# Performance work log

Measured on AMD Instinct MI355X. Metric: run time of the kernel, lower is better.

## Reference

```python
import jax, jax.numpy as jnp
import numpy as np

B = 8          # batch_size
N = 2048       # N_particles
D_SP = 2       # spatial dims
D = 16         # D_SP + hidden_dim
K = 32         # max_num_neighbors
R = 0.08       # neighbor_radius
DT = 0.01      # leapfrog step
BIG = 1e9


def setup_inputs() -> dict:
    key = jax.random.key(0)
    ks = jax.random.split(key, 8)
    H, C = 64, 32
    # node state: small random hidden features, deterministic disk positions
    x = jax.random.normal(ks[0], (B * N, D), dtype=jnp.float32) * 0.001
    i = jnp.arange(N, dtype=jnp.float32)
    golden = jnp.pi * (3.0 - jnp.sqrt(5.0))
    theta = i * golden
    r = 0.6 * jnp.sqrt((i + 0.5) / N)
    pos = jnp.stack([r * jnp.cos(theta), r * jnp.sin(theta)], axis=1)  # [N,2]
    pos = jnp.tile(pos, (B, 1)) + 0.01 * jax.random.normal(ks[1], (B * N, 2), dtype=jnp.float32)
    x = x.at[:, :D_SP].set(pos)
    W1 = jax.random.normal(ks[2], (2 * D, H), dtype=jnp.float32) * (1.0 / np.sqrt(2 * D))
    b1 = jnp.zeros((H,), jnp.float32)
    W2 = jax.random.normal(ks[3], (H, C), dtype=jnp.float32) * (1.0 / np.sqrt(H))
    b2 = jnp.zeros((C,), jnp.float32)
    Wout = jax.random.normal(ks[4], (C, 1), dtype=jnp.float32) * (1.0 / np.sqrt(C))
    bout = jnp.zeros((1,), jnp.float32)
    batch = jnp.repeat(jnp.arange(B, dtype=jnp.int64), N)
    return {"x": x, "W1": W1, "b1": b1, "W2": W2, "b2": b2,
            "Wout": Wout, "bout": bout, "batch": batch, "steps": 2}


def reference(x, W1, b1, W2, b2, Wout, bout, batch, steps):
    Bn, Df = x.shape
    Bc = int(np.asarray(batch)[-1]) + 1      # batch is contiguous blocks
    Nn = Bn // Bc
    eye = jnp.eye(Nn, dtype=x.dtype) * BIG   # no self-loops (loop=False)

    def hamiltonian(xv):
        xb = xv.reshape(Bc, Nn, Df)
        pos = xb[:, :, :D_SP]                              # [B,N,2]
        # radius_graph: pairwise sq-dist per simulation, capped at K neighbors
        d2 = jnp.sum((pos[:, :, None, :] - pos[:, None, :, :]) ** 2, axis=-1)  # [B,N,N]
        d2 = d2 + eye
        negd, idx = jax.lax.top_k(-d2, K)                  # K nearest per node
        valid = (-negd) < (R * R)                          # [B,N,K]
        # gather neighbor states (HNNConv message on concat(x_i, x_j))
        xj = xb[jnp.arange(Bc)[:, None, None], idx]        # [B,N,K,D]
        xi = jnp.broadcast_to(xb[:, :, None, :], xj.shape)
        m = jnp.tanh(jnp.concatenate([xi, xj], axis=-1) @ W1 + b1)  # [B,N,K,H]
        m = m @ W2 + b2                                    # [B,N,K,C]
        m = jnp.where(valid[..., None], m, 0.0)
        agg = m.sum(axis=2)                                # sum aggregation [B,N,C]
        h = agg @ Wout + bout                              # per-node Hamiltonian [B,N,1]
        return h.sum()

    for _ in range(int(steps)):
        dHdx = jax.grad(hamiltonian)(x)
        x = x - DT * dHdx
    return x
```

## Files before the change

### kernel.cpp

```cpp
#include <hip/hip_runtime.h>
#include <cstdint>
#include <cstddef>

#define BB   8
#define NN   2048
#define DD   16
#define HHH  64
#define KK   32
#define CAP  96
#define FCAP 48
#define DT_C 0.01f
#define R2_C (0.08f * 0.08f)
#define CEXP (-2.885390081777927f)

#define GRID 17
#define NCEL (GRID * GRID)
#define GOFF 0.68f
#define CINV 12.5f
#define CSTRIDE 320

#define WPB   8
#define BLOCK (WPB * 64)

__device__ __forceinline__ float dist2(float px, float py, float qx, float qy) {
    float dx = __fsub_rn(px, qx);
    float dy = __fsub_rn(py, qy);
    return __fadd_rn(__fmul_rn(dx, dx), __fmul_rn(dy, dy));
}

__device__ __forceinline__ int prefix_cnt(unsigned long long m) {
    return (int)__builtin_amdgcn_mbcnt_hi(
        (unsigned)(m >> 32), __builtin_amdgcn_mbcnt_lo((unsigned)m, 0u));
}

__device__ __forceinline__ int swizzled_slot(int blk, int w, int& bbase) {
    bbase = (blk & 7) << 11;
    return (blk >> 3) * WPB + w;
}

__device__ __forceinline__ int clampi(int v, int lo, int hi) {
    return v < lo ? lo : (v > hi ? hi : v);
}

template <bool FIRST>
__global__ __launch_bounds__(1024) void k_bin(
    const float* __restrict__ x, const float* __restrict__ pos,
    const float* __restrict__ W2, const float* __restrict__ Wout,
    float2* __restrict__ sortedPos, unsigned short* __restrict__ sortedIdx,
    int* __restrict__ cellStart, float* __restrict__ vOut) {
    __shared__ int hist[NCEL], base[NCEL + 1], cursor[NCEL];
    int bat = blockIdx.x, bbase = bat << 11, tid = threadIdx.x;
    if (tid < NCEL) hist[tid] = 0;
    if (blockIdx.x == 0 && tid >= 512 && tid < 512 + HHH) {
        int hh = tid - 512;
        float acc = 0.f;
        for (int c = 0; c < 32; c++) acc = fmaf(W2[hh * 32 + c], Wout[c], acc);
        vOut[hh] = acc;
    }
    __syncthreads();
    float2 q[2]; int cid[2];
#pragma unroll
    for (int u = 0; u < 2; ++u) {
        int i = tid + (u << 10);
        float2 qq = FIRST ? *(const float2*)(x + (size_t)(bbase + i) * DD)
                          : *(const float2*)(pos + (size_t)(bbase + i) * 2);
        q[u] = qq;
        int cx = clampi((int)((qq.x + GOFF) * CINV), 0, GRID - 1);
        int cy = clampi((int)((qq.y + GOFF) * CINV), 0, GRID - 1);
        cid[u] = cy * GRID + cx;
        atomicAdd(&hist[cid[u]], 1);
    }
    __syncthreads();
    if (tid < 64) {
        int loc[5], s = 0;
#pragma unroll
        for (int k = 0; k < 5; ++k) {
            int idx = tid * 5 + k;
            loc[k] = (idx < NCEL) ? hist[idx] : 0;
            s += loc[k];
        }
        int pre = s;
#pragma unroll
        for (int off = 1; off < 64; off <<= 1) {
            int t = __shfl_up(pre, off);
            if (tid >= off) pre += t;
        }
        pre -= s;
#pragma unroll
        for (int k = 0; k < 5; ++k) {
            int idx = tid * 5 + k;
            if (idx <= NCEL) base[idx] = pre;
            pre += loc[k];
        }
    }
    __syncthreads();
    if (tid < NCEL) cursor[tid] = base[tid];
    if (tid <= NCEL) cellStart[bat * CSTRIDE + tid] = base[tid];
    __syncthreads();
#pragma unroll
    for (int u = 0; u < 2; ++u) {
        int dst = atomicAdd(&cursor[cid[u]], 1);
        sortedPos[bbase + dst] = q[u];
        sortedIdx[bbase + dst] = (unsigned short)(tid + (u << 10));
    }
}

__global__ __launch_bounds__(BLOCK) void k_neighbors(
    const float* __restrict__ x,
    const float2* __restrict__ sortedPos, const unsigned short* __restrict__ sortedIdx,
    const int* __restrict__ cellStart, const float* __restrict__ W1,
    float2* __restrict__ candList, unsigned short* __restrict__ fwdList,
    int* __restrict__ cntArr, float* __restrict__ cutArr,
    float* __restrict__ Aplane, float* __restrict__ Dplane) {
    __shared__ float2 sDJ[WPB][CAP];

    int tid = threadIdx.x;
    int w = tid >> 6, lane = tid & 63;
    int bbase;
    int s = swizzled_slot(blockIdx.x, w, bbase);
    int bat = bbase >> 11;
    int gs = bbase + s;

    int jol = (int)sortedIdx[gs];
    const float* xrow = x + (size_t)(bbase + jol) * DD;
    float xv = (lane < DD) ? xrow[lane] : 0.f;
    float px = __shfl(xv, 0), py = __shfl(xv, 1);
    float A = 0.f, Dv = 0.f;
#pragma unroll
    for (int f = 0; f < DD; f++) {
        float xf = __shfl(xv, f);
        A  = fmaf(xf, W1[f * HHH + lane], A);
        Dv = fmaf(xf, W1[(DD + f) * HHH + lane], Dv);
    }
    Aplane[((size_t)gs << 6) + lane] = A;
    Dplane[((size_t)gs << 6) + lane] = Dv;

    const int* CS = cellStart + bat * CSTRIDE;
    int cx = clampi((int)((px + GOFF) * CINV), 0, GRID - 1);
    int cy = clampi((int)((py + GOFF) * CINV), 0, GRID - 1);
    int xlo = cx > 0 ? cx - 1 : 0;
    int xhi = cx < GRID - 1 ? cx + 1 : GRID - 1;
    int rs0 = 0, rl0 = 0, rs1 = 0, rl1 = 0, rs2 = 0, rl2 = 0;
    if (cy > 0) {
        int a = CS[(cy - 1) * GRID + xlo], b = CS[(cy - 1) * GRID + xhi + 1];
        rs0 = a; rl0 = b - a;
    }
    {
        int a = CS[cy * GRID + xlo], b = CS[cy * GRID + xhi + 1];
        rs1 = a; rl1 = b - a;
    }
    if (cy < GRID - 1) {
        int a = CS[(cy + 1) * GRID + xlo], b = CS[(cy + 1) * GRID + xhi + 1];
        rs2 = a; rl2 = b - a;
    }
    int tot = rl0 + rl1 + rl2;

    int cnt = 0;
    for (int c0 = 0; c0 < tot; c0 += 64) {
        int t = c0 + lane;
        int j = rs0 + t;
        int u1 = t - rl0;
        if (u1 >= 0) j = rs1 + u1;
        int u2 = u1 - rl1;
        if (u2 >= 0) j = rs2 + u2;
        bool in = t < tot;
        float2 q = sortedPos[bbase + (in ? j : 0)];
        float d2 = dist2(px, py, q.x, q.y);
        bool hit = in && (d2 < R2_C);
        unsigned long long m = __ballot(hit);
        int idx = cnt + prefix_cnt(m);
        if (hit && idx < CAP)
            sDJ[w][idx] = make_float2(d2, __uint_as_float((unsigned)j));
        cnt += (int)__popcll(m);
    }
    if (cnt > CAP) cnt = CAP;
    __threadfence_block();

    float cutoff = R2_C;
    if (cnt > KK + 1) {
        const float INF = 1e30f;
        if (cnt <= 64) {
            float v = (lane < cnt) ? sDJ[w][lane].x : INF;
#pragma unroll
            for (int k = 2; k <= 64; k <<= 1) {
#pragma unroll
                for (int j = k >> 1; j > 0; j >>= 1) {
                    float pv = __shfl_xor(v, j);
                    bool up = ((lane & k) == 0);
                    bool takeMin = (((lane & j) == 0) == up);
                    v = takeMin ? fminf(v, pv) : fmaxf(v, pv);
                }
            }
            cutoff = __shfl(v, KK);
        } else {
            float e0 = (lane < cnt) ? sDJ[w][lane].x : INF;
            float e1 = (lane + 64 < cnt) ? sDJ[w][lane + 64].x : INF;
            int r0 = 0, q0 = 0, r1 = 0, q1 = 0;
            for (int k = 0; k < cnt; k++) {
                float val = sDJ[w][k].x;
                r0 += (val < e0); q0 += (val == e0);
                r1 += (val < e1); q1 += (val == e1);
            }
            bool c0 = (r0 <= KK) && (r0 + q0 > KK);
            bool c1 = (r1 <= KK) && (r1 + q1 > KK);
            float cand = c0 ? e0 : (c1 ? e1 : INF);
#pragma unroll
            for (int off = 32; off; off >>= 1) cand = fminf(cand, __shfl_xor(cand, off));
            cutoff = cand;
        }
    }

    int me = 0, mf = 0;
    for (int c0 = 0; c0 < cnt; c0 += 64) {
        int c = c0 + lane;
        bool act = c < cnt;
        float2 e = sDJ[w][act ? c : 0];
        unsigned js = __float_as_uint(e.y);
        bool keep = act && ((int)js != s);
        unsigned long long mK = __ballot(keep);
        int ie = me + prefix_cnt(mK);
        if (keep) candList[(size_t)gs * CAP + ie] = e;
        me += (int)__popcll(mK);
        bool fw = keep && (e.x <= cutoff);
        unsigned long long mF = __ballot(fw);
        int iF = mf + prefix_cnt(mF);
        if (fw && iF < FCAP) fwdList[(size_t)gs * FCAP + iF] = (unsigned short)js;
        mf += (int)__popcll(mF);
    }
    if (mf > FCAP) mf = FCAP;
    if (lane == 0) { cutArr[gs] = cutoff; cntArr[gs] = me | (mf << 16); }
}

__global__ __launch_bounds__(BLOCK) void k_grad(
    const float* __restrict__ x, const unsigned short* __restrict__ sortedIdx,
    const float* __restrict__ cutArr, const int* __restrict__ cntArr,
    const float2* __restrict__ candList, const unsigned short* __restrict__ fwdList,
    const float* __restrict__ Aplane, const float* __restrict__ Dplane,
    const float* __restrict__ W1, const float* __restrict__ b1,
    const float* __restrict__ vArr,
    float* __restrict__ xOut, float* __restrict__ posOut) {
    __shared__ float sW1t[HHH * 33];
    __shared__ alignas(16) unsigned short sFwd[WPB][FCAP];
    __shared__ alignas(16) unsigned short sRev[WPB][CAP];
    __shared__ float sS[WPB][128];

    int tid = threadIdx.x;
    int w = tid >> 6, h = tid & 63;
    int bbase;
    int s = swizzled_slot(blockIdx.x, w, bbase);
    int gs = bbase + s;

    for (int t = tid; t < 2 * DD * HHH; t += BLOCK) {
        int f = t >> 6, hh = t & 63;
        sW1t[hh * 33 + f] = W1[t];
    }
    __syncthreads();

    float b1h = b1[h];
    float Apb = Aplane[((size_t)gs << 6) + h] + b1h;
    float Dpb = Dplane[((size_t)gs << 6) + h] + b1h;
    float vh4 = 4.f * vArr[h];
    int packed = cntArr[gs];
    int cnt = packed & 0xffff;
    int mf = packed >> 16;

    if (h < mf) sFwd[w][h] = fwdList[(size_t)gs * FCAP + h];

    int mr = 0;
    for (int c0 = 0; c0 < cnt; c0 += 64) {
        int c = c0 + h;
        bool act = c < cnt;
        float2 e = candList[(size_t)gs * CAP + (act ? c : 0)];
        unsigned jl = __float_as_uint(e.y) & (NN - 1);
        bool rev = act && (e.x <= cutArr[bbase + jl]);
        unsigned long long mR = __ballot(rev);
        int iR = mr + prefix_cnt(mR);
        if (rev) sRev[w][iR] = (unsigned short)jl;
        mr += (int)__popcll(mR);
    }
    __threadfence_block();

    const float* baseD = Dplane + ((size_t)bbase << 6);
    const float* baseA = Aplane + ((size_t)bbase << 6);
    float T1 = 0.f, T2 = 0.f;

    auto s2core = [&](float z) {
        float a = __builtin_amdgcn_exp2f(CEXP * fabsf(z));
        float bb = 1.f + a;
        return a * __builtin_amdgcn_rcpf(bb * bb);
    };

#define UNPACK8(Q0, Q1, U)                                            \
    unsigned U[8];                                                    \
    U[0] = (unsigned)__builtin_amdgcn_readfirstlane(Q0.x);            \
    U[1] = (unsigned)__builtin_amdgcn_readfirstlane(Q0.y);            \
    U[2] = (unsigned)__builtin_amdgcn_readfirstlane(Q0.z);            \
    U[3] = (unsigned)__builtin_amdgcn_readfirstlane(Q0.w);            \
    U[4] = (unsigned)__builtin_amdgcn_readfirstlane(Q1.x);            \
    U[5] = (unsigned)__builtin_amdgcn_readfirstlane(Q1.y);            \
    U[6] = (unsigned)__builtin_amdgcn_readfirstlane(Q1.z);            \
    U[7] = (unsigned)__builtin_amdgcn_readfirstlane(Q1.w);

    {
        const unsigned short* L = sFwd[w];
        int c = 0;
        for (; c + 16 <= mf; c += 16) {
            int4 q0 = *(const int4*)(L + c);
            int4 q1 = *(const int4*)(L + c + 8);
            UNPACK8(q0, q1, u)
            float d[16];
#pragma unroll
            for (int k = 0; k < 8; ++k) {
                d[2 * k]     = baseD[((size_t)(u[k] & 0xffffu) << 6) + h];
                d[2 * k + 1] = baseD[((size_t)(u[k] >> 16) << 6) + h];
            }
#pragma unroll
            for (int k = 0; k < 16; ++k) T1 += s2core(Apb + d[k]);
        }
        for (; c + 8 <= mf; c += 8) {
            int4 q0 = *(const int4*)(L + c);
            int4 q1 = q0;
            UNPACK8(q0, q1, u)
            float d[8];
#pragma unroll
            for (int k = 0; k < 4; ++k) {
                d[2 * k]     = baseD[((size_t)(u[k] & 0xffffu) << 6) + h];
                d[2 * k + 1] = baseD[((size_t)(u[k] >> 16) << 6) + h];
            }
#pragma unroll
            for (int k = 0; k < 8; ++k) T1 += s2core(Apb + d[k]);
        }
        for (; c < mf; ++c) {
            unsigned jl = (unsigned)__builtin_amdgcn_readfirstlane((int)L[c]);
            T1 += s2core(Apb + baseD[((size_t)jl << 6) + h]);
        }
    }
    {
        const unsigned short* L = sRev[w];
        int c = 0;
        for (; c + 16 <= mr; c += 16) {
            int4 q0 = *(const int4*)(L + c);
            int4 q1 = *(const int4*)(L + c + 8);
            UNPACK8(q0, q1, u)
            float d[16];
#pragma unroll
            for (int k = 0; k < 8; ++k) {
                d[2 * k]     = baseA[((size_t)(u[k] & 0xffffu) << 6) + h];
                d[2 * k + 1] = baseA[((size_t)(u[k] >> 16) << 6) + h];
            }
#pragma unroll
            for (int k = 0; k < 16; ++k) T2 += s2core(Dpb + d[k]);
        }
        for (; c + 8 <= mr; c += 8) {
            int4 q0 = *(const int4*)(L + c);
            int4 q1 = q0;
            UNPACK8(q0, q1, u)
            float d[8];
#pragma unroll
            for (int k = 0; k < 4; ++k) {
                d[2 * k]     = baseA[((size_t)(u[k] & 0xffffu) << 6) + h];
                d[2 * k + 1] = baseA[((size_t)(u[k] >> 16) << 6) + h];
            }
#pragma unroll
            for (int k = 0; k < 8; ++k) T2 += s2core(Dpb + d[k]);
        }
        for (; c < mr; ++c) {
            unsigned jl = (unsigned)__builtin_amdgcn_readfirstlane((int)L[c]);
            T2 += s2core(Dpb + baseA[((size_t)jl << 6) + h]);
        }
    }
#undef UNPACK8

    sS[w][h] = vh4 * T1;
    sS[w][64 + h] = vh4 * T2;
    __threadfence_block();

    float g = 0.f;
    if (h < 32) {
        const float* Sv = &sS[w][(h < 16) ? 0 : 64];
        float a0 = 0.f, a1 = 0.f, a2 = 0.f, a3 = 0.f;
        for (int hh = 0; hh < 64; hh += 4) {
            a0 = fmaf(sW1t[(hh + 0) * 33 + h], Sv[hh + 0], a0);
            a1 = fmaf(sW1t[(hh + 1) * 33 + h], Sv[hh + 1], a1);
            a2 = fmaf(sW1t[(hh + 2) * 33 + h], Sv[hh + 2], a2);
            a3 = fmaf(sW1t[(hh + 3) * 33 + h], Sv[hh + 3], a3);
        }
        g = (a0 + a1) + (a2 + a3);
    }
    float g2 = __shfl(g, (h + 16) & 63);
    int jo = (int)sortedIdx[gs];
    if (h < DD) {
        size_t prow = (size_t)(bbase + jo) * DD;
        float xn = x[prow + h] - DT_C * (g + g2);
        xOut[prow + h] = xn;
        if (h < 2) posOut[(bbase + jo) * 2 + h] = xn;
    }
}

extern "C" void kernel_launch(void* const* d_in, const int* in_sizes, int n_in,
                              void* d_out, int out_size, void* d_ws, size_t ws_size,
                              hipStream_t stream) {
    const float* x0   = (const float*)d_in[0];
    const float* W1   = (const float*)d_in[1];
    const float* b1   = (const float*)d_in[2];
    const float* W2   = (const float*)d_in[3];
    const float* Wout = (const float*)d_in[5];
    float* out = (float*)d_out;

    float* ws   = (float*)d_ws;
    float* posA = ws;
    float* posB = posA + 32768;
    float* x1   = posB + 32768;
    float* Apl  = x1 + 262144;
    float* Dpl  = Apl + 16384 * 64;
    float* cut  = Dpl + 16384 * 64;
    int*   cnt  = (int*)(cut + 16384);
    float2* cand = (float2*)(cnt + 16384);
    unsigned short* fwd = (unsigned short*)(cand + (size_t)16384 * CAP);
    float2* sPosS = (float2*)(fwd + (size_t)16384 * FCAP);
    unsigned short* sIdx = (unsigned short*)(sPosS + 16384);
    int* cellStart = (int*)(sIdx + 16384);
    float* vArr = (float*)(cellStart + BB * CSTRIDE);

    const int NB = (BB * NN) / WPB;

    k_bin<true><<<BB, 1024, 0, stream>>>(x0, nullptr, W2, Wout, sPosS, sIdx,
                                         cellStart, vArr);
    k_neighbors<<<NB, BLOCK, 0, stream>>>(x0, sPosS, sIdx, cellStart, W1,
                                          cand, fwd, cnt, cut, Apl, Dpl);
    k_grad<<<NB, BLOCK, 0, stream>>>(x0, sIdx, cut, cnt, cand, fwd, Apl, Dpl,
                                     W1, b1, vArr, x1, posB);
    k_bin<false><<<BB, 1024, 0, stream>>>(nullptr, posB, W2, Wout, sPosS, sIdx,
                                          cellStart, vArr);
    k_neighbors<<<NB, BLOCK, 0, stream>>>(x1, sPosS, sIdx, cellStart, W1,
                                          cand, fwd, cnt, cut, Apl, Dpl);
    k_grad<<<NB, BLOCK, 0, stream>>>(x1, sIdx, cut, cnt, cand, fwd, Apl, Dpl,
                                     W1, b1, vArr, out, posA);
}
```

Measured before the change: 167.4 us.

## Recompute neighbor window in grad kernel instead of storing candidate lists

The neighbor kernel now only computes the per-node K-th-neighbor cutoff and the projected planes, and no longer writes candidate and forward lists to global memory. The grad kernel rescans the 3x3 cell window itself, building forward and reverse lists in shared memory from positions and cutoffs. The exp2 scale constant is also folded into the stored A/D planes so the sigmoid-derivative core skips one multiply. This trades a second spatial scan for removing the large candList/fwdList global writes and reads.

```diff
diff --git a/kernel.cpp b/kernel.cpp
--- a/kernel.cpp
+++ b/kernel.cpp
@@ -40,6 +40,38 @@
 
 __device__ __forceinline__ int clampi(int v, int lo, int hi) {
     return v < lo ? lo : (v > hi ? hi : v);
+}
+
+struct Win { int rs0, rl0, rs1, rl1, rs2, rl2, tot; };
+__device__ __forceinline__ Win cell_window(const int* CS, float px, float py) {
+    Win W;
+    int cx = clampi((int)((px + GOFF) * CINV), 0, GRID - 1);
+    int cy = clampi((int)((py + GOFF) * CINV), 0, GRID - 1);
+    int xlo = cx > 0 ? cx - 1 : 0;
+    int xhi = cx < GRID - 1 ? cx + 1 : GRID - 1;
+    W.rs0 = 0; W.rl0 = 0; W.rs2 = 0; W.rl2 = 0;
+    if (cy > 0) {
+        int a = CS[(cy - 1) * GRID + xlo], b = CS[(cy - 1) * GRID + xhi + 1];
+        W.rs0 = a; W.rl0 = b - a;
+    }
+    {
+        int a = CS[cy * GRID + xlo], b = CS[cy * GRID + xhi + 1];
+        W.rs1 = a; W.rl1 = b - a;
+    }
+    if (cy < GRID - 1) {
+        int a = CS[(cy + 1) * GRID + xlo], b = CS[(cy + 1) * GRID + xhi + 1];
+        W.rs2 = a; W.rl2 = b - a;
+    }
+    W.tot = W.rl0 + W.rl1 + W.rl2;
+    return W;
+}
+__device__ __forceinline__ int win_map(const Win& W, int t) {
+    int j = W.rs0 + t;
+    int u1 = t - W.rl0;
+    if (u1 >= 0) j = W.rs1 + u1;
+    int u2 = u1 - W.rl1;
+    if (u2 >= 0) j = W.rs2 + u2;
+    return j;
 }
 
 template <bool FIRST>
@@ -105,14 +137,13 @@
     }
 }
 
-__global__ __launch_bounds__(BLOCK) void k_neighbors(
+__global__ __launch_bounds__(BLOCK) void k_cut(
     const float* __restrict__ x,
     const float2* __restrict__ sortedPos, const unsigned short* __restrict__ sortedIdx,
     const int* __restrict__ cellStart, const float* __restrict__ W1,
-    float2* __restrict__ candList, unsigned short* __restrict__ fwdList,
-    int* __restrict__ cntArr, float* __restrict__ cutArr,
-    float* __restrict__ Aplane, float* __restrict__ Dplane) {
-    __shared__ float2 sDJ[WPB][CAP];
+    float* __restrict__ cutArr,
+    float* __restrict__ Asp, float* __restrict__ Dsp) {
+    __shared__ float sD[WPB][CAP];
 
     int tid = threadIdx.x;
     int w = tid >> 6, lane = tid & 63;
@@ -132,45 +163,22 @@
         A  = fmaf(xf, W1[f * HHH + lane], A);
         Dv = fmaf(xf, W1[(DD + f) * HHH + lane], Dv);
     }
-    Aplane[((size_t)gs << 6) + lane] = A;
-    Dplane[((size_t)gs << 6) + lane] = Dv;
+    Asp[((size_t)gs << 6) + lane] = CEXP * A;
+    Dsp[((size_t)gs << 6) + lane] = CEXP * Dv;
 
     const int* CS = cellStart + bat * CSTRIDE;
-    int cx = clampi((int)((px + GOFF) * CINV), 0, GRID - 1);
-    int cy = clampi((int)((py + GOFF) * CINV), 0, GRID - 1);
-    int xlo = cx > 0 ? cx - 1 : 0;
-    int xhi = cx < GRID - 1 ? cx + 1 : GRID - 1;
-    int rs0 = 0, rl0 = 0, rs1 = 0, rl1 = 0, rs2 = 0, rl2 = 0;
-    if (cy > 0) {
-        int a = CS[(cy - 1) * GRID + xlo], b = CS[(cy - 1) * GRID + xhi + 1];
-        rs0 = a; rl0 = b - a;
-    }
-    {
-        int a = CS[cy * GRID + xlo], b = CS[cy * GRID + xhi + 1];
-        rs1 = a; rl1 = b - a;
-    }
-    if (cy < GRID - 1) {
-        int a = CS[(cy + 1) * GRID + xlo], b = CS[(cy + 1) * GRID + xhi + 1];
-        rs2 = a; rl2 = b - a;
-    }
-    int tot = rl0 + rl1 + rl2;
-
+    Win W = cell_window(CS, px, py);
     int cnt = 0;
-    for (int c0 = 0; c0 < tot; c0 += 64) {
+    for (int c0 = 0; c0 < W.tot; c0 += 64) {
         int t = c0 + lane;
-        int j = rs0 + t;
-        int u1 = t - rl0;
-        if (u1 >= 0) j = rs1 + u1;
-        int u2 = u1 - rl1;
-        if (u2 >= 0) j = rs2 + u2;
-        bool in = t < tot;
+        int j = win_map(W, t);
+        bool in = t < W.tot;
         float2 q = sortedPos[bbase + (in ? j : 0)];
         float d2 = dist2(px, py, q.x, q.y);
         bool hit = in && (d2 < R2_C);
         unsigned long long m = __ballot(hit);
         int idx = cnt + prefix_cnt(m);
-        if (hit && idx < CAP)
-            sDJ[w][idx] = make_float2(d2, __uint_as_float((unsigned)j));
+        if (hit && idx < CAP) sD[w][idx] = d2;
         cnt += (int)__popcll(m);
     }
     if (cnt > CAP) cnt = CAP;
@@ -180,7 +188,7 @@
     if (cnt > KK + 1) {
         const float INF = 1e30f;
         if (cnt <= 64) {
-            float v = (lane < cnt) ? sDJ[w][lane].x : INF;
+            float v = (lane < cnt) ? sD[w][lane] : INF;
 #pragma unroll
             for (int k = 2; k <= 64; k <<= 1) {
 #pragma unroll
@@ -193,11 +201,11 @@
             }
             cutoff = __shfl(v, KK);
         } else {
-            float e0 = (lane < cnt) ? sDJ[w][lane].x : INF;
-            float e1 = (lane + 64 < cnt) ? sDJ[w][lane + 64].x : INF;
+            float e0 = (lane < cnt) ? sD[w][lane] : INF;
+            float e1 = (lane + 64 < cnt) ? sD[w][lane + 64] : INF;
             int r0 = 0, q0 = 0, r1 = 0, q1 = 0;
             for (int k = 0; k < cnt; k++) {
-                float val = sDJ[w][k].x;
+                float val = sD[w][k];
                 r0 += (val < e0); q0 += (val == e0);
                 r1 += (val < e1); q1 += (val == e1);
             }
@@ -209,33 +217,14 @@
             cutoff = cand;
         }
     }
-
-    int me = 0, mf = 0;
-    for (int c0 = 0; c0 < cnt; c0 += 64) {
-        int c = c0 + lane;
-        bool act = c < cnt;
-        float2 e = sDJ[w][act ? c : 0];
-        unsigned js = __float_as_uint(e.y);
-        bool keep = act && ((int)js != s);
-        unsigned long long mK = __ballot(keep);
-        int ie = me + prefix_cnt(mK);
-        if (keep) candList[(size_t)gs * CAP + ie] = e;
-        me += (int)__popcll(mK);
-        bool fw = keep && (e.x <= cutoff);
-        unsigned long long mF = __ballot(fw);
-        int iF = mf + prefix_cnt(mF);
-        if (fw && iF < FCAP) fwdList[(size_t)gs * FCAP + iF] = (unsigned short)js;
-        mf += (int)__popcll(mF);
-    }
-    if (mf > FCAP) mf = FCAP;
-    if (lane == 0) { cutArr[gs] = cutoff; cntArr[gs] = me | (mf << 16); }
+    if (lane == 0) cutArr[gs] = cutoff;
 }
 
 __global__ __launch_bounds__(BLOCK) void k_grad(
     const float* __restrict__ x, const unsigned short* __restrict__ sortedIdx,
-    const float* __restrict__ cutArr, const int* __restrict__ cntArr,
-    const float2* __restrict__ candList, const unsigned short* __restrict__ fwdList,
-    const float* __restrict__ Aplane, const float* __restrict__ Dplane,
+    const float2* __restrict__ sortedPos, const int* __restrict__ cellStart,
+    const float* __restrict__ cutArr,
+    const float* __restrict__ Asp, const float* __restrict__ Dsp,
     const float* __restrict__ W1, const float* __restrict__ b1,
     const float* __restrict__ vArr,
     float* __restrict__ xOut, float* __restrict__ posOut) {
@@ -248,6 +237,7 @@
     int w = tid >> 6, h = tid & 63;
     int bbase;
     int s = swizzled_slot(blockIdx.x, w, bbase);
+    int bat = bbase >> 11;
     int gs = bbase + s;
 
     for (int t = tid; t < 2 * DD * HHH; t += BLOCK) {
@@ -256,36 +246,48 @@
     }
     __syncthreads();
 
-    float b1h = b1[h];
-    float Apb = Aplane[((size_t)gs << 6) + h] + b1h;
-    float Dpb = Dplane[((size_t)gs << 6) + h] + b1h;
+    float b1s = CEXP * b1[h];
+    float Apbs = Asp[((size_t)gs << 6) + h] + b1s;
+    float Dpbs = Dsp[((size_t)gs << 6) + h] + b1s;
     float vh4 = 4.f * vArr[h];
-    int packed = cntArr[gs];
-    int cnt = packed & 0xffff;
-    int mf = packed >> 16;
-
-    if (h < mf) sFwd[w][h] = fwdList[(size_t)gs * FCAP + h];
-
-    int mr = 0;
-    for (int c0 = 0; c0 < cnt; c0 += 64) {
-        int c = c0 + h;
-        bool act = c < cnt;
-        float2 e = candList[(size_t)gs * CAP + (act ? c : 0)];
-        unsigned jl = __float_as_uint(e.y) & (NN - 1);
-        bool rev = act && (e.x <= cutArr[bbase + jl]);
-        unsigned long long mR = __ballot(rev);
+
+    float2 pp = sortedPos[gs];
+    float px = pp.x, py = pp.y;
+    float cutp = cutArr[gs];
+
+    const int* CS = cellStart + bat * CSTRIDE;
+    Win W = cell_window(CS, px, py);
+    int mf = 0, mr = 0;
+    for (int c0 = 0; c0 < W.tot; c0 += 64) {
+        int t = c0 + h;
+        int j = win_map(W, t);
+        bool in = t < W.tot;
+        int ja = in ? j : 0;
+        float2 q = sortedPos[bbase + ja];
+        float cutj = cutArr[bbase + ja];
+        float d2 = dist2(px, py, q.x, q.y);
+        bool hit = in && (d2 < R2_C) && (j != s);
+        bool fw = hit && (d2 <= cutp);
+        bool rv = hit && (d2 <= cutj);
+        unsigned long long mF = __ballot(fw);
+        int iF = mf + prefix_cnt(mF);
+        if (fw && iF < FCAP) sFwd[w][iF] = (unsigned short)j;
+        mf += (int)__popcll(mF);
+        unsigned long long mR = __ballot(rv);
         int iR = mr + prefix_cnt(mR);
-        if (rev) sRev[w][iR] = (unsigned short)jl;
+        if (rv && iR < CAP) sRev[w][iR] = (unsigned short)j;
         mr += (int)__popcll(mR);
     }
+    if (mf > FCAP) mf = FCAP;
+    if (mr > CAP) mr = CAP;
     __threadfence_block();
 
-    const float* baseD = Dplane + ((size_t)bbase << 6);
-    const float* baseA = Aplane + ((size_t)bbase << 6);
+    const float* baseD = Dsp + ((size_t)bbase << 6);
+    const float* baseA = Asp + ((size_t)bbase << 6);
     float T1 = 0.f, T2 = 0.f;
 
-    auto s2core = [&](float z) {
-        float a = __builtin_amdgcn_exp2f(CEXP * fabsf(z));
+    auto s2core = [&](float wz) {
+        float a = __builtin_amdgcn_exp2f(-fabsf(wz));
         float bb = 1.f + a;
         return a * __builtin_amdgcn_rcpf(bb * bb);
     };
@@ -311,11 +313,13 @@
             float d[16];
 #pragma unroll
             for (int k = 0; k < 8; ++k) {
-                d[2 * k]     = baseD[((size_t)(u[k] & 0xffffu) << 6) + h];
-                d[2 * k + 1] = baseD[((size_t)(u[k] >> 16) << 6) + h];
-            }
-#pragma unroll
-            for (int k = 0; k < 16; ++k) T1 += s2core(Apb + d[k]);
+                const float* ra = baseD + ((size_t)(u[k] & 0xffffu) << 6);
+                const float* rb = baseD + ((size_t)(u[k] >> 16) << 6);
+                d[2 * k]     = ra[h];
+                d[2 * k + 1] = rb[h];
+            }
+#pragma unroll
+            for (int k = 0; k < 16; ++k) T1 += s2core(Apbs + d[k]);
         }
         for (; c + 8 <= mf; c += 8) {
             int4 q0 = *(const int4*)(L + c);
@@ -324,15 +328,17 @@
             float d[8];
 #pragma unroll
             for (int k = 0; k < 4; ++k) {
-                d[2 * k]     = baseD[((size_t)(u[k] & 0xffffu) << 6) + h];
-                d[2 * k + 1] = baseD[((size_t)(u[k] >> 16) << 6) + h];
-            }
-#pragma unroll
-            for (int k = 0; k < 8; ++k) T1 += s2core(Apb + d[k]);
+                const float* ra = baseD + ((size_t)(u[k] & 0xffffu) << 6);
+                const float* rb = baseD + ((size_t)(u[k] >> 16) << 6);
+                d[2 * k]     = ra[h];
+                d[2 * k + 1] = rb[h];
+            }
+#pragma unroll
+            for (int k = 0; k < 8; ++k) T1 += s2core(Apbs + d[k]);
         }
         for (; c < mf; ++c) {
             unsigned jl = (unsigned)__builtin_amdgcn_readfirstlane((int)L[c]);
-            T1 += s2core(Apb + baseD[((size_t)jl << 6) + h]);
+            T1 += s2core(Apbs + (baseD + ((size_t)jl << 6))[h]);
         }
     }
     {
@@ -345,11 +351,13 @@
             float d[16];
 #pragma unroll
             for (int k = 0; k < 8; ++k) {
-                d[2 * k]     = baseA[((size_t)(u[k] & 0xffffu) << 6) + h];
-                d[2 * k + 1] = baseA[((size_t)(u[k] >> 16) << 6) + h];
-            }
-#pragma unroll
-            for (int k = 0; k < 16; ++k) T2 += s2core(Dpb + d[k]);
+                const float* ra = baseA + ((size_t)(u[k] & 0xffffu) << 6);
+                const float* rb = baseA + ((size_t)(u[k] >> 16) << 6);
+                d[2 * k]     = ra[h];
+                d[2 * k + 1] = rb[h];
+            }
+#pragma unroll
+            for (int k = 0; k < 16; ++k) T2 += s2core(Dpbs + d[k]);
         }
         for (; c + 8 <= mr; c += 8) {
             int4 q0 = *(const int4*)(L + c);
@@ -358,15 +366,17 @@
             float d[8];
 #pragma unroll
             for (int k = 0; k < 4; ++k) {
-                d[2 * k]     = baseA[((size_t)(u[k] & 0xffffu) << 6) + h];
-                d[2 * k + 1] = baseA[((size_t)(u[k] >> 16) << 6) + h];
-            }
-#pragma unroll
-            for (int k = 0; k < 8; ++k) T2 += s2core(Dpb + d[k]);
+                const float* ra = baseA + ((size_t)(u[k] & 0xffffu) << 6);
+                const float* rb = baseA + ((size_t)(u[k] >> 16) << 6);
+                d[2 * k]     = ra[h];
+                d[2 * k + 1] = rb[h];
+            }
+#pragma unroll
+            for (int k = 0; k < 8; ++k) T2 += s2core(Dpbs + d[k]);
         }
         for (; c < mr; ++c) {
             unsigned jl = (unsigned)__builtin_amdgcn_readfirstlane((int)L[c]);
-            T2 += s2core(Dpb + baseA[((size_t)jl << 6) + h]);
+            T2 += s2core(Dpbs + (baseA + ((size_t)jl << 6))[h]);
         }
     }
 #undef UNPACK8
@@ -411,13 +421,10 @@
     float* posA = ws;
     float* posB = posA + 32768;
     float* x1   = posB + 32768;
-    float* Apl  = x1 + 262144;
-    float* Dpl  = Apl + 16384 * 64;
-    float* cut  = Dpl + 16384 * 64;
-    int*   cnt  = (int*)(cut + 16384);
-    float2* cand = (float2*)(cnt + 16384);
-    unsigned short* fwd = (unsigned short*)(cand + (size_t)16384 * CAP);
-    float2* sPosS = (float2*)(fwd + (size_t)16384 * FCAP);
+    float* Asp  = x1 + 262144;
+    float* Dsp  = Asp + 16384 * 64;
+    float* cut  = Dsp + 16384 * 64;
+    float2* sPosS = (float2*)(cut + 16384);
     unsigned short* sIdx = (unsigned short*)(sPosS + 16384);
     int* cellStart = (int*)(sIdx + 16384);
     float* vArr = (float*)(cellStart + BB * CSTRIDE);
@@ -426,14 +433,12 @@
 
     k_bin<true><<<BB, 1024, 0, stream>>>(x0, nullptr, W2, Wout, sPosS, sIdx,
                                          cellStart, vArr);
-    k_neighbors<<<NB, BLOCK, 0, stream>>>(x0, sPosS, sIdx, cellStart, W1,
-                                          cand, fwd, cnt, cut, Apl, Dpl);
-    k_grad<<<NB, BLOCK, 0, stream>>>(x0, sIdx, cut, cnt, cand, fwd, Apl, Dpl,
+    k_cut<<<NB, BLOCK, 0, stream>>>(x0, sPosS, sIdx, cellStart, W1, cut, Asp, Dsp);
+    k_grad<<<NB, BLOCK, 0, stream>>>(x0, sIdx, sPosS, cellStart, cut, Asp, Dsp,
                                      W1, b1, vArr, x1, posB);
     k_bin<false><<<BB, 1024, 0, stream>>>(nullptr, posB, W2, Wout, sPosS, sIdx,
                                           cellStart, vArr);
-    k_neighbors<<<NB, BLOCK, 0, stream>>>(x1, sPosS, sIdx, cellStart, W1,
-                                          cand, fwd, cnt, cut, Apl, Dpl);
-    k_grad<<<NB, BLOCK, 0, stream>>>(x1, sIdx, cut, cnt, cand, fwd, Apl, Dpl,
+    k_cut<<<NB, BLOCK, 0, stream>>>(x1, sPosS, sIdx, cellStart, W1, cut, Asp, Dsp);
+    k_grad<<<NB, BLOCK, 0, stream>>>(x1, sIdx, sPosS, cellStart, cut, Asp, Dsp,
                                      W1, b1, vArr, out, posA);
 }
```

Measured after the change: 159.4 us. 4.7% less time.
